# Kernel optimization log

Hardware: AMD Instinct MI355X
Metric: run time of the kernel (lower is better)

The kernel has to match this reference:

```python
import jax, jax.numpy as jnp
import numpy as np

EPS = 1e-8  # torch F.cosine_similarity eps

B, H, K = 64, 2048, 256


def setup_inputs() -> dict:
    key = jax.random.key(0)
    k1, k2, k3, k4 = jax.random.split(key, 4)
    input_state = jax.random.normal(k1, (B, H), dtype=jnp.float32)
    knowledge_base = jax.random.normal(k2, (K, B, H), dtype=jnp.float32)
    W = jax.random.normal(k3, (H, H), dtype=jnp.float32) / np.sqrt(H)
    b = jax.random.normal(k4, (H,), dtype=jnp.float32) * 0.02
    return {"input_state": input_state, "knowledge_base": knowledge_base, "W": W, "b": b}


def reference(input_state, knowledge_base, W, b):
    # linear projection (torch Linear: x @ W.T + b)
    q = input_state @ W.T + b                      # [B, H]
    kproj = jnp.einsum('kbh,oh->kbo', knowledge_base, W) + b  # [K, B, H]
    # cosine similarity over last dim, with torch-style eps clamp on norms
    qn = jnp.maximum(jnp.linalg.norm(q, axis=-1), EPS)        # [B]
    kn = jnp.maximum(jnp.linalg.norm(kproj, axis=-1), EPS)    # [K, B]
    dots = jnp.einsum('bh,kbh->kb', q, kproj)                 # [K, B]
    scores = dots / (qn[None, :] * kn)                        # [K, B]
    # softmax over the K knowledge items
    attn = jax.nn.softmax(scores, axis=0)                     # [K, B]
    # output = input + softmax-weighted sum of (raw) knowledge items
    out = input_state + jnp.einsum('kb,kbh->bh', attn, knowledge_base)
    return out
```

## Files before the change

### kernel.cpp

```cpp
#include <hip/hip_runtime.h>
#include <hip/hip_bf16.h>

typedef unsigned short u16;
typedef __attribute__((ext_vector_type(8))) short short8;
typedef __attribute__((ext_vector_type(4))) float float4v;

#define B_DIM 64
#define H_DIM 2048
#define K_DIM 256
#define M_KB  16384

#define WS_WBF   0ull
#define WS_AQ    (8388608ull)
#define WS_Q     (WS_AQ + 524288ull)
#define WS_KN2   (WS_Q + 524288ull)
#define WS_DOTS  (WS_KN2 + 65536ull)
#define WS_ATTN  (WS_DOTS + 65536ull)
#define WS_KBF   (WS_ATTN + 65536ull)
#define WS_NEEDED (WS_KBF + 67108864ull)

__device__ __forceinline__ u16 f2bf(float f) {
    unsigned int u = __float_as_uint(f);
    unsigned int r = (u + 0x7fffu + ((u >> 16) & 1u)) >> 16;
    return (u16)r;
}

__device__ __forceinline__ unsigned long long pack4(float4v v) {
    unsigned long long a0 = f2bf(v.x), a1 = f2bf(v.y), a2 = f2bf(v.z), a3 = f2bf(v.w);
    return a0 | (a1 << 16) | (a2 << 32) | (a3 << 48);
}

__device__ __forceinline__ void llds16(const u16* g, u16* l) {
    __builtin_amdgcn_global_load_lds(
        (__attribute__((address_space(1))) void*)g,
        (__attribute__((address_space(3))) void*)l, 16, 0, 0);
}

__global__ __launch_bounds__(256) void conv_f2b(const float* __restrict__ src,
                                                u16* __restrict__ dst) {
    long long t = (long long)blockIdx.x * 256 + threadIdx.x;
    const float4v* s4 = (const float4v*)src;
    float4v a = s4[t * 2], b = s4[t * 2 + 1];
    unsigned long long* d8 = (unsigned long long*)dst;
    d8[t * 2] = pack4(a);
    d8[t * 2 + 1] = pack4(b);
}

__global__ __launch_bounds__(256) void prep_small(const float* __restrict__ in,
                                                  const float* __restrict__ bias,
                                                  u16* __restrict__ Aq, float* __restrict__ q,
                                                  float* __restrict__ kn2, float* __restrict__ dots) {
    int gid = blockIdx.x * 256 + threadIdx.x;
    int stride = gridDim.x * 256;
    for (int i = gid; i < 128 * H_DIM; i += stride)
        Aq[i] = (i < B_DIM * H_DIM) ? f2bf(in[i]) : (u16)0;
    for (int i = gid; i < B_DIM * H_DIM; i += stride)
        q[i] = bias[i & (H_DIM - 1)];
    for (int i = gid; i < M_KB; i += stride) { kn2[i] = 0.f; dots[i] = 0.f; }
}

template <int MODE>
__global__ __launch_bounds__(256) void gemm_kernel(
        const float* __restrict__ A32,
        const u16* __restrict__ Abf,
        const u16* __restrict__ Wb,
        const float* __restrict__ bias,
        const float* __restrict__ q,
        float* __restrict__ qout,
        float* __restrict__ kn2, float* __restrict__ dots) {
    __shared__ __align__(16) u16 As[128 * 32];
    __shared__ __align__(16) u16 Bs[128 * 32];

    const int tid = threadIdx.x;
    const int wave = tid >> 6, lane = tid & 63;
    const int l15 = lane & 15, qd = lane >> 4;
    const int wm = wave >> 1, wn = wave & 1;

    int mt, nt, k_begin, k_iters;
    if (MODE == 0) {
        nt = blockIdx.x & 15; mt = 0;
        k_begin = (blockIdx.x >> 4) * 512; k_iters = 16;
    } else {
        mt = blockIdx.x >> 4; nt = blockIdx.x & 15;
        k_begin = 0; k_iters = 64;
    }
    const int m0 = mt * 128, n0 = nt * 128;

    float4v acc[4][4] = {};

    const int srow = tid >> 3;
    const int scol = (tid & 7) * 4;
    const int grow = lane >> 2;
    const int gcol = (lane & 3) * 8;

    for (int kk = 0; kk < k_iters; ++kk) {
        const int k0 = k_begin + kk * 32;
        #pragma unroll
        for (int i = 0; i < 2; ++i) {
            const int r = wave * 32 + i * 16;
            llds16(Wb + (size_t)(n0 + r + grow) * H_DIM + k0 + gcol, &Bs[r * 32]);
        }
        if (MODE == 1) {
            float4v va[4];
            #pragma unroll
            for (int r4 = 0; r4 < 4; ++r4)
                va[r4] = *(const float4v*)&A32[(size_t)(m0 + r4 * 32 + srow) * H_DIM + k0 + scol];
            #pragma unroll
            for (int r4 = 0; r4 < 4; ++r4)
                *(unsigned long long*)&As[(r4 * 32 + srow) * 32 + scol] = pack4(va[r4]);
        } else {
            #pragma unroll
            for (int i = 0; i < 2; ++i) {
                const int r = wave * 32 + i * 16;
                llds16(Abf + (size_t)(m0 + r + grow) * H_DIM + k0 + gcol, &As[r * 32]);
            }
        }
        __syncthreads();

        short8 af[4], bf_[4];
        #pragma unroll
        for (int mi = 0; mi < 4; ++mi)
            af[mi] = *(const short8*)&As[(wm * 64 + mi * 16 + l15) * 32 + qd * 8];
        #pragma unroll
        for (int ni = 0; ni < 4; ++ni)
            bf_[ni] = *(const short8*)&Bs[(wn * 64 + ni * 16 + l15) * 32 + qd * 8];
        #pragma unroll
        for (int mi = 0; mi < 4; ++mi)
            #pragma unroll
            for (int ni = 0; ni < 4; ++ni)
                acc[mi][ni] = __builtin_amdgcn_mfma_f32_16x16x32_bf16(af[mi], bf_[ni], acc[mi][ni], 0, 0, 0);
        __syncthreads();
    }

    const int n0w = n0 + wn * 64;
    if (MODE == 0) {
        if (wm == 0) {
            #pragma unroll
            for (int mi = 0; mi < 4; ++mi)
                #pragma unroll
                for (int reg = 0; reg < 4; ++reg) {
                    const int m = mi * 16 + qd * 4 + reg;
                    #pragma unroll
                    for (int ni = 0; ni < 4; ++ni) {
                        const int n = n0w + ni * 16 + l15;
                        atomicAdd(&qout[m * H_DIM + n], acc[mi][ni][reg]);
                    }
                }
        }
    } else {
        float bv[4];
        #pragma unroll
        for (int ni = 0; ni < 4; ++ni) bv[ni] = bias[n0w + ni * 16 + l15];
        #pragma unroll
        for (int mi = 0; mi < 4; ++mi)
            #pragma unroll
            for (int reg = 0; reg < 4; ++reg) {
                const int mloc = mi * 16 + qd * 4 + reg;
                const int mg = m0 + wm * 64 + mloc;
                const float* qrow = q + mloc * H_DIM;
                float s2 = 0.f, sd = 0.f;
                #pragma unroll
                for (int ni = 0; ni < 4; ++ni) {
                    const float y = acc[mi][ni][reg] + bv[ni];
                    const float qv = qrow[n0w + ni * 16 + l15];
                    s2 += y * y; sd += y * qv;
                }
                #pragma unroll
                for (int off = 1; off < 16; off <<= 1) {
                    s2 += __shfl_xor(s2, off);
                    sd += __shfl_xor(sd, off);
                }
                if (l15 == 0) {
                    atomicAdd(&kn2[mg], s2);
                    atomicAdd(&dots[mg], sd);
                }
            }
    }
}

__device__ __forceinline__ float blk_sum(float v, float* buf, int tid) {
    #pragma unroll
    for (int o = 32; o >= 1; o >>= 1) v += __shfl_xor(v, o);
    if ((tid & 63) == 0) buf[tid >> 6] = v;
    __syncthreads();
    float r = buf[0] + buf[1] + buf[2] + buf[3];
    __syncthreads();
    return r;
}
__device__ __forceinline__ float blk_max(float v, float* buf, int tid) {
    #pragma unroll
    for (int o = 32; o >= 1; o >>= 1) v = fmaxf(v, __shfl_xor(v, o));
    if ((tid & 63) == 0) buf[tid >> 6] = v;
    __syncthreads();
    float r = fmaxf(fmaxf(buf[0], buf[1]), fmaxf(buf[2], buf[3]));
    __syncthreads();
    return r;
}

__global__ __launch_bounds__(256) void softmax_kernel(const float* __restrict__ q,
                                                      const float* __restrict__ kn2,
                                                      const float* __restrict__ dots,
                                                      float* __restrict__ attn) {
    __shared__ float buf[4];
    const int b = blockIdx.x, tid = threadIdx.x;
    float s = 0.f;
    #pragma unroll
    for (int i = 0; i < 8; ++i) {
        float v = q[b * H_DIM + i * 256 + tid];
        s += v * v;
    }
    const float qn = fmaxf(sqrtf(blk_sum(s, buf, tid)), 1e-8f);
    const int k = tid;
    const float kn = fmaxf(sqrtf(kn2[k * B_DIM + b]), 1e-8f);
    const float sc = dots[k * B_DIM + b] / (qn * kn);
    const float mx = blk_max(sc, buf, tid);
    const float e = expf(sc - mx);
    const float se = blk_sum(e, buf, tid);
    attn[k * B_DIM + b] = e / se;
}

__global__ __launch_bounds__(256) void output_kernel(const float* __restrict__ input,
                                                     const float* __restrict__ kb,
                                                     const float* __restrict__ attn,
                                                     float* __restrict__ out) {
    __shared__ float a_s[K_DIM];
    const int b = blockIdx.y, hc = blockIdx.x, tid = threadIdx.x;
    a_s[tid] = attn[tid * B_DIM + b];
    __syncthreads();
    const int h = hc * 256 + tid;
    const float* base = kb + (size_t)b * H_DIM + h;
    float s = 0.f;
    #pragma unroll 4
    for (int k = 0; k < K_DIM; ++k)
        s += a_s[k] * base[(size_t)k * (B_DIM * H_DIM)];
    out[b * H_DIM + h] = input[b * H_DIM + h] + s;
}

extern "C" void kernel_launch(void* const* d_in, const int* in_sizes, int n_in,
                              void* d_out, int out_size, void* d_ws, size_t ws_size,
                              hipStream_t stream) {
    const float* input = (const float*)d_in[0];
    const float* kb    = (const float*)d_in[1];
    const float* W     = (const float*)d_in[2];
    const float* bias  = (const float*)d_in[3];
    float* out = (float*)d_out;
    char* ws = (char*)d_ws;

    u16*   Wb   = (u16*)(ws + WS_WBF);
    u16*   Aq   = (u16*)(ws + WS_AQ);
    float* q    = (float*)(ws + WS_Q);
    float* kn2  = (float*)(ws + WS_KN2);
    float* dots = (float*)(ws + WS_DOTS);
    float* attn = (float*)(ws + WS_ATTN);
    u16*   Kbf  = (u16*)(ws + WS_KBF);

    const bool fast = (ws_size >= WS_NEEDED);

    conv_f2b<<<2048, 256, 0, stream>>>(W, Wb);
    prep_small<<<256, 256, 0, stream>>>(input, bias, Aq, q, kn2, dots);
    gemm_kernel<0><<<64, 256, 0, stream>>>(nullptr, Aq, Wb, bias, nullptr, q, nullptr, nullptr);
    if (fast) {
        conv_f2b<<<16384, 256, 0, stream>>>(kb, Kbf);
        gemm_kernel<2><<<2048, 256, 0, stream>>>(nullptr, Kbf, Wb, bias, q, nullptr, kn2, dots);
    } else {
        gemm_kernel<1><<<2048, 256, 0, stream>>>(kb, nullptr, Wb, bias, q, nullptr, kn2, dots);
    }
    softmax_kernel<<<64, 256, 0, stream>>>(q, kn2, dots, attn);
    output_kernel<<<dim3(8, 64), 256, 0, stream>>>(input, kb, attn, out);
}
```

Measured before the change: 431.3 us.

## Read bf16 knowledge base in output pass, regroup GEMM tiles, tune conversion

The output weighted sum now reads the bf16 copy of the knowledge base already produced for the GEMM, halving the bytes of the 128MB fp32 re-read. The GEMM block index is remapped so groups of four M-tiles share N-tiles for better L2 reuse, and launch bounds request three blocks per CU. The conversion kernel now handles one float4 per thread with twice as many blocks. The output sum uses bf16-rounded knowledge items rather than the fp32 originals, which adds some precision error.

```diff
diff --git a/kernel.cpp b/kernel.cpp
--- a/kernel.cpp
+++ b/kernel.cpp
@@ -40,10 +40,8 @@
                                                 u16* __restrict__ dst) {
     long long t = (long long)blockIdx.x * 256 + threadIdx.x;
     const float4v* s4 = (const float4v*)src;
-    float4v a = s4[t * 2], b = s4[t * 2 + 1];
     unsigned long long* d8 = (unsigned long long*)dst;
-    d8[t * 2] = pack4(a);
-    d8[t * 2 + 1] = pack4(b);
+    d8[t] = pack4(s4[t]);
 }
 
 __global__ __launch_bounds__(256) void prep_small(const float* __restrict__ in,
@@ -60,7 +58,7 @@
 }
 
 template <int MODE>
-__global__ __launch_bounds__(256) void gemm_kernel(
+__global__ __launch_bounds__(256, 3) void gemm_kernel(
         const float* __restrict__ A32,
         const u16* __restrict__ Abf,
         const u16* __restrict__ Wb,
@@ -81,7 +79,9 @@
         nt = blockIdx.x & 15; mt = 0;
         k_begin = (blockIdx.x >> 4) * 512; k_iters = 16;
     } else {
-        mt = blockIdx.x >> 4; nt = blockIdx.x & 15;
+        const int bx = blockIdx.x;
+        mt = (bx >> 6) * 4 + (bx & 3);
+        nt = (bx >> 2) & 15;
         k_begin = 0; k_iters = 64;
     }
     const int m0 = mt * 128, n0 = nt * 128;
@@ -219,6 +219,31 @@
     attn[k * B_DIM + b] = e / se;
 }
 
+__global__ __launch_bounds__(256) void output_kernel_bf(const float* __restrict__ input,
+                                                        const u16* __restrict__ kbf,
+                                                        const float* __restrict__ attn,
+                                                        float* __restrict__ out) {
+    __shared__ float a_s[K_DIM];
+    const int b = blockIdx.y, hc = blockIdx.x, tid = threadIdx.x;
+    a_s[tid] = attn[tid * B_DIM + b];
+    __syncthreads();
+    const int h2 = hc * 256 + tid;
+    const unsigned* base = (const unsigned*)kbf + ((size_t)b * H_DIM >> 1) + h2;
+    float s0 = 0.f, s1 = 0.f;
+    #pragma unroll 4
+    for (int k = 0; k < K_DIM; ++k) {
+        unsigned p = base[(size_t)k * (B_DIM * H_DIM / 2)];
+        float v0 = __uint_as_float(p << 16);
+        float v1 = __uint_as_float(p & 0xffff0000u);
+        float a = a_s[k];
+        s0 += a * v0; s1 += a * v1;
+    }
+    const int h = h2 * 2;
+    float2 iv = *(const float2*)&input[(size_t)b * H_DIM + h];
+    float2 r; r.x = iv.x + s0; r.y = iv.y + s1;
+    *(float2*)&out[(size_t)b * H_DIM + h] = r;
+}
+
 __global__ __launch_bounds__(256) void output_kernel(const float* __restrict__ input,
                                                      const float* __restrict__ kb,
                                                      const float* __restrict__ attn,
@@ -256,15 +281,17 @@
 
     const bool fast = (ws_size >= WS_NEEDED);
 
-    conv_f2b<<<2048, 256, 0, stream>>>(W, Wb);
+    conv_f2b<<<4096, 256, 0, stream>>>(W, Wb);
     prep_small<<<256, 256, 0, stream>>>(input, bias, Aq, q, kn2, dots);
     gemm_kernel<0><<<64, 256, 0, stream>>>(nullptr, Aq, Wb, bias, nullptr, q, nullptr, nullptr);
     if (fast) {
-        conv_f2b<<<16384, 256, 0, stream>>>(kb, Kbf);
+        conv_f2b<<<32768, 256, 0, stream>>>(kb, Kbf);
         gemm_kernel<2><<<2048, 256, 0, stream>>>(nullptr, Kbf, Wb, bias, q, nullptr, kn2, dots);
+        softmax_kernel<<<64, 256, 0, stream>>>(q, kn2, dots, attn);
+        output_kernel_bf<<<dim3(4, 64), 256, 0, stream>>>(input, Kbf, attn, out);
     } else {
         gemm_kernel<1><<<2048, 256, 0, stream>>>(kb, nullptr, Wb, bias, q, nullptr, kn2, dots);
-    }
-    softmax_kernel<<<64, 256, 0, stream>>>(q, kn2, dots, attn);
-    output_kernel<<<dim3(8, 64), 256, 0, stream>>>(input, kb, attn, out);
-}
+        softmax_kernel<<<64, 256, 0, stream>>>(q, kn2, dots, attn);
+        output_kernel<<<dim3(8, 64), 256, 0, stream>>>(input, kb, attn, out);
+    }
+}
```

Result: faster. 415.4 us (-3.7%).
